# Optimization experiments

Hardware: AMD Instinct MI355X
Metric: run time of the kernel (lower is better)

Reference implementation:

```python
import jax, jax.numpy as jnp
import numpy as np

LAMBD = 100.0

def setup_inputs() -> dict:
    key = jax.random.key(0)
    k1, k2, k3 = jax.random.split(key, 3)
    shape = (4096, 4096)
    resnet_outputs = jax.random.normal(k1, shape, dtype=jnp.float32)
    gru_outputs = jax.random.normal(k2, shape, dtype=jnp.float32)
    target = jax.random.normal(k3, shape, dtype=jnp.float32)
    return {"resnet_outputs": resnet_outputs, "gru_outputs": gru_outputs, "target": target}

def reference(resnet_outputs, gru_outputs, target):
    # L1 loss (mean absolute error)
    l1 = jnp.mean(jnp.abs(resnet_outputs - target))
    # smooth_loss: mean absolute deviation of flattened gru_outputs
    g = gru_outputs.ravel()
    smooth = jnp.mean(jnp.abs(g - jnp.mean(g)))
    return l1 + LAMBD * smooth
```

## Files before the change

kernel.cpp:

```cpp
#include <hip/hip_runtime.h>


typedef float f32x4 __attribute__((ext_vector_type(4)));

#define LAMBD 100.0
#define BLOCK 256
#define PT 8
#define TILE (BLOCK * PT)

__device__ __forceinline__ void block_reduce2(float a, float g, float* oa, float* og) {
    #pragma unroll
    for (int off = 32; off; off >>= 1) {
        a += __shfl_down(a, off);
        g += __shfl_down(g, off);
    }
    __shared__ float la[4], lg[4];
    int w = threadIdx.x >> 6;
    if ((threadIdx.x & 63) == 0) { la[w] = a; lg[w] = g; }
    __syncthreads();
    if (threadIdx.x == 0) {
        float ra = 0.f, rg = 0.f;
        #pragma unroll
        for (int i = 0; i < 4; ++i) { ra += la[i]; rg += lg[i]; }
        *oa = ra; *og = rg;
    }
}

__device__ __forceinline__ int swizzle_bid(int bid, int nb) {
    if ((nb & 7) == 0) {
        int nx = nb >> 3;
        return (bid & 7) * nx + (bid >> 3);
    }
    return bid;
}

__global__ void __launch_bounds__(BLOCK) pass1_kernel(const f32x4* __restrict__ r,
                                                      const f32x4* __restrict__ t,
                                                      const f32x4* __restrict__ g,
                                                      double* __restrict__ ws,
                                                      int n4, int nb) {
    int swz = swizzle_bid(blockIdx.x, nb);
    long base = (long)swz * TILE + threadIdx.x;
    float s_abs = 0.f, s_g = 0.f;

    if ((long)swz * TILE + TILE <= n4) {
        f32x4 rv[PT], tv[PT], gv[PT];
        #pragma unroll
        for (int k = 0; k < PT; ++k) rv[k] = __builtin_nontemporal_load(&r[base + k * BLOCK]);
        #pragma unroll
        for (int k = 0; k < PT; ++k) tv[k] = __builtin_nontemporal_load(&t[base + k * BLOCK]);
        #pragma unroll
        for (int k = 0; k < PT; ++k) gv[k] = g[base + k * BLOCK];
        #pragma unroll
        for (int k = 0; k < PT; ++k) {
            f32x4 d = rv[k] - tv[k];
            s_abs += fabsf(d.x) + fabsf(d.y) + fabsf(d.z) + fabsf(d.w);
            s_g   += (gv[k].x + gv[k].y) + (gv[k].z + gv[k].w);
        }
    } else {
        for (int k = 0; k < PT; ++k) {
            long i = base + (long)k * BLOCK;
            if (i < n4) {
                f32x4 rv = r[i], tv = t[i], gv = g[i];
                s_abs += fabsf(rv.x - tv.x) + fabsf(rv.y - tv.y) +
                         fabsf(rv.z - tv.z) + fabsf(rv.w - tv.w);
                s_g += (gv.x + gv.y) + (gv.z + gv.w);
            }
        }
    }

    float ba, bg;
    block_reduce2(s_abs, s_g, &ba, &bg);
    if (threadIdx.x == 0) {
        ws[swz]      = (double)ba;
        ws[nb + swz] = (double)bg;
    }
}

__global__ void __launch_bounds__(1024) mean_kernel(double* __restrict__ ws, int nb, double inv_n) {
    double v = 0.0;
    for (int i = threadIdx.x; i < nb; i += 1024) v += ws[nb + i];
    #pragma unroll
    for (int off = 32; off; off >>= 1) v += __shfl_down(v, off);
    __shared__ double lds[16];
    int w = threadIdx.x >> 6;
    if ((threadIdx.x & 63) == 0) lds[w] = v;
    __syncthreads();
    if (threadIdx.x == 0) {
        double s = 0.0;
        #pragma unroll
        for (int i = 0; i < 16; ++i) s += lds[i];
        ws[2 * nb] = s * inv_n;
    }
}

__global__ void __launch_bounds__(BLOCK) pass2_kernel(const f32x4* __restrict__ g,
                                                      double* __restrict__ ws,
                                                      int n4, int nb, int p2off) {
    float m = (float)ws[2 * nb];
    int swz = swizzle_bid(blockIdx.x, nb);
    long base = (long)swz * TILE + threadIdx.x;
    float s = 0.f;

    if ((long)swz * TILE + TILE <= n4) {
        f32x4 gv[PT];
        #pragma unroll
        for (int k = 0; k < PT; ++k) gv[k] = g[base + k * BLOCK];
        #pragma unroll
        for (int k = 0; k < PT; ++k) {
            s += fabsf(gv[k].x - m) + fabsf(gv[k].y - m) +
                 fabsf(gv[k].z - m) + fabsf(gv[k].w - m);
        }
    } else {
        for (int k = 0; k < PT; ++k) {
            long i = base + (long)k * BLOCK;
            if (i < n4) {
                f32x4 gv = g[i];
                s += fabsf(gv.x - m) + fabsf(gv.y - m) +
                     fabsf(gv.z - m) + fabsf(gv.w - m);
            }
        }
    }

    float bs, dummy;
    block_reduce2(s, 0.f, &bs, &dummy);
    if (threadIdx.x == 0) ws[p2off + swz] = (double)bs;
}

__global__ void __launch_bounds__(1024) finalize_kernel(const double* __restrict__ ws,
                                                        float* __restrict__ out,
                                                        int nb, int p2off, double inv_n) {
    double a = 0.0, s = 0.0;
    for (int i = threadIdx.x; i < nb; i += 1024) { a += ws[i]; s += ws[p2off + i]; }
    #pragma unroll
    for (int off = 32; off; off >>= 1) {
        a += __shfl_down(a, off);
        s += __shfl_down(s, off);
    }
    __shared__ double la[16], ls[16];
    int w = threadIdx.x >> 6;
    if ((threadIdx.x & 63) == 0) { la[w] = a; ls[w] = s; }
    __syncthreads();
    if (threadIdx.x == 0) {
        double ra = 0.0, rs = 0.0;
        #pragma unroll
        for (int i = 0; i < 16; ++i) { ra += la[i]; rs += ls[i]; }
        out[0] = (float)(ra * inv_n + LAMBD * (rs * inv_n));
    }
}

extern "C" void kernel_launch(void* const* d_in, const int* in_sizes, int n_in,
                              void* d_out, int out_size, void* d_ws, size_t ws_size,
                              hipStream_t stream) {
    const f32x4* r = (const f32x4*)d_in[0];
    const f32x4* g = (const f32x4*)d_in[1];
    const f32x4* t = (const f32x4*)d_in[2];
    float* out = (float*)d_out;
    double* ws = (double*)d_ws;

    int n = in_sizes[0];
    int n4 = n >> 2;
    int nb = (n4 + TILE - 1) / TILE;
    int p2off = 2 * nb + 64;
    double inv_n = 1.0 / (double)n;

    pass1_kernel<<<nb, BLOCK, 0, stream>>>(r, t, g, ws, n4, nb);
    mean_kernel<<<1, 1024, 0, stream>>>(ws, nb, inv_n);
    pass2_kernel<<<nb, BLOCK, 0, stream>>>(g, ws, n4, nb, p2off);
    finalize_kernel<<<1, 1024, 0, stream>>>(ws, out, nb, p2off, inv_n);
}
```

Measured before the change: 198.7 us.

## Fuse four reduction kernels into one cooperative persistent kernel with grid syncs

Replaces the pass1, mean, pass2 and finalize kernels with a single cooperative kernel. It runs a persistent grid sized from the occupancy query times 256 CUs, loops over tiles, and uses grid.sync between phases. Every block computes the mean itself from the workspace partials. This removes three kernel launches and their gaps. The cost is grid-wide barrier overhead and a smaller grid of persistent blocks, so the gru tensor may no longer sit in cache for the second pass in the same way as before.

```diff
diff --git a/kernel.cpp b/kernel.cpp
--- a/kernel.cpp
+++ b/kernel.cpp
@@ -1,5 +1,8 @@
 #include <hip/hip_runtime.h>
+#include <hip/hip_cooperative_groups.h>
 
+
+namespace cg = cooperative_groups;
 
 typedef float f32x4 __attribute__((ext_vector_type(4)));
 
@@ -8,144 +11,134 @@
 #define PT 8
 #define TILE (BLOCK * PT)
 
-__device__ __forceinline__ void block_reduce2(float a, float g, float* oa, float* og) {
-    #pragma unroll
-    for (int off = 32; off; off >>= 1) {
-        a += __shfl_down(a, off);
-        g += __shfl_down(g, off);
+__device__ __forceinline__ int swizzle_tile(int tile, int ntiles) {
+    if ((ntiles & 7) == 0) {
+        int nx = ntiles >> 3;
+        return (tile & 7) * nx + (tile >> 3);
     }
-    __shared__ float la[4], lg[4];
-    int w = threadIdx.x >> 6;
-    if ((threadIdx.x & 63) == 0) { la[w] = a; lg[w] = g; }
-    __syncthreads();
-    if (threadIdx.x == 0) {
-        float ra = 0.f, rg = 0.f;
-        #pragma unroll
-        for (int i = 0; i < 4; ++i) { ra += la[i]; rg += lg[i]; }
-        *oa = ra; *og = rg;
-    }
+    return tile;
 }
 
-__device__ __forceinline__ int swizzle_bid(int bid, int nb) {
-    if ((nb & 7) == 0) {
-        int nx = nb >> 3;
-        return (bid & 7) * nx + (bid >> 3);
-    }
-    return bid;
-}
+__global__ void __launch_bounds__(BLOCK, 8)
+fused_kernel(const f32x4* __restrict__ r, const f32x4* __restrict__ t,
+             const f32x4* __restrict__ g, double* __restrict__ ws,
+             float* __restrict__ out, int n4, int ntiles, double inv_n) {
+    cg::grid_group grid = cg::this_grid();
+    __shared__ float  lfa[4], lfb[4];
+    __shared__ double lda[8];
+    const int nblk = gridDim.x;
+    const int tid  = threadIdx.x;
 
-__global__ void __launch_bounds__(BLOCK) pass1_kernel(const f32x4* __restrict__ r,
-                                                      const f32x4* __restrict__ t,
-                                                      const f32x4* __restrict__ g,
-                                                      double* __restrict__ ws,
-                                                      int n4, int nb) {
-    int swz = swizzle_bid(blockIdx.x, nb);
-    long base = (long)swz * TILE + threadIdx.x;
     float s_abs = 0.f, s_g = 0.f;
-
-    if ((long)swz * TILE + TILE <= n4) {
-        f32x4 rv[PT], tv[PT], gv[PT];
-        #pragma unroll
-        for (int k = 0; k < PT; ++k) rv[k] = __builtin_nontemporal_load(&r[base + k * BLOCK]);
-        #pragma unroll
-        for (int k = 0; k < PT; ++k) tv[k] = __builtin_nontemporal_load(&t[base + k * BLOCK]);
-        #pragma unroll
-        for (int k = 0; k < PT; ++k) gv[k] = g[base + k * BLOCK];
-        #pragma unroll
-        for (int k = 0; k < PT; ++k) {
-            f32x4 d = rv[k] - tv[k];
-            s_abs += fabsf(d.x) + fabsf(d.y) + fabsf(d.z) + fabsf(d.w);
-            s_g   += (gv[k].x + gv[k].y) + (gv[k].z + gv[k].w);
-        }
-    } else {
-        for (int k = 0; k < PT; ++k) {
-            long i = base + (long)k * BLOCK;
-            if (i < n4) {
-                f32x4 rv = r[i], tv = t[i], gv = g[i];
-                s_abs += fabsf(rv.x - tv.x) + fabsf(rv.y - tv.y) +
-                         fabsf(rv.z - tv.z) + fabsf(rv.w - tv.w);
-                s_g += (gv.x + gv.y) + (gv.z + gv.w);
+    for (int tile = blockIdx.x; tile < ntiles; tile += nblk) {
+        int swz = swizzle_tile(tile, ntiles);
+        long base = (long)swz * TILE + tid;
+        if ((long)swz * TILE + TILE <= n4) {
+            f32x4 rv[PT], tv[PT], gv[PT];
+            #pragma unroll
+            for (int k = 0; k < PT; ++k) rv[k] = __builtin_nontemporal_load(&r[base + k * BLOCK]);
+            #pragma unroll
+            for (int k = 0; k < PT; ++k) tv[k] = __builtin_nontemporal_load(&t[base + k * BLOCK]);
+            #pragma unroll
+            for (int k = 0; k < PT; ++k) gv[k] = g[base + k * BLOCK];
+            #pragma unroll
+            for (int k = 0; k < PT; ++k) {
+                f32x4 d = rv[k] - tv[k];
+                s_abs += fabsf(d.x) + fabsf(d.y) + fabsf(d.z) + fabsf(d.w);
+                s_g   += (gv[k].x + gv[k].y) + (gv[k].z + gv[k].w);
+            }
+        } else {
+            for (int k = 0; k < PT; ++k) {
+                long i = base + (long)k * BLOCK;
+                if (i < n4) {
+                    f32x4 rv = r[i], tv = t[i], gv = g[i];
+                    s_abs += fabsf(rv.x - tv.x) + fabsf(rv.y - tv.y) +
+                             fabsf(rv.z - tv.z) + fabsf(rv.w - tv.w);
+                    s_g += (gv.x + gv.y) + (gv.z + gv.w);
+                }
             }
         }
     }
+    #pragma unroll
+    for (int off = 32; off; off >>= 1) {
+        s_abs += __shfl_down(s_abs, off);
+        s_g   += __shfl_down(s_g, off);
+    }
+    if ((tid & 63) == 0) { lfa[tid >> 6] = s_abs; lfb[tid >> 6] = s_g; }
+    __syncthreads();
+    if (tid == 0) {
+        float ba = lfa[0] + lfa[1] + lfa[2] + lfa[3];
+        float bg = lfb[0] + lfb[1] + lfb[2] + lfb[3];
+        ws[blockIdx.x]        = (double)ba;
+        ws[nblk + blockIdx.x] = (double)bg;
+        __threadfence();
+    }
+    grid.sync();
 
-    float ba, bg;
-    block_reduce2(s_abs, s_g, &ba, &bg);
-    if (threadIdx.x == 0) {
-        ws[swz]      = (double)ba;
-        ws[nb + swz] = (double)bg;
-    }
-}
-
-__global__ void __launch_bounds__(1024) mean_kernel(double* __restrict__ ws, int nb, double inv_n) {
     double v = 0.0;
-    for (int i = threadIdx.x; i < nb; i += 1024) v += ws[nb + i];
+    for (int i = tid; i < nblk; i += BLOCK) v += ws[nblk + i];
     #pragma unroll
     for (int off = 32; off; off >>= 1) v += __shfl_down(v, off);
-    __shared__ double lds[16];
-    int w = threadIdx.x >> 6;
-    if ((threadIdx.x & 63) == 0) lds[w] = v;
+    if ((tid & 63) == 0) lda[tid >> 6] = v;
     __syncthreads();
-    if (threadIdx.x == 0) {
-        double s = 0.0;
-        #pragma unroll
-        for (int i = 0; i < 16; ++i) s += lds[i];
-        ws[2 * nb] = s * inv_n;
-    }
-}
+    if (tid == 0) lda[4] = (lda[0] + lda[1] + lda[2] + lda[3]) * inv_n;
+    __syncthreads();
+    const float m = (float)lda[4];
 
-__global__ void __launch_bounds__(BLOCK) pass2_kernel(const f32x4* __restrict__ g,
-                                                      double* __restrict__ ws,
-                                                      int n4, int nb, int p2off) {
-    float m = (float)ws[2 * nb];
-    int swz = swizzle_bid(blockIdx.x, nb);
-    long base = (long)swz * TILE + threadIdx.x;
-    float s = 0.f;
-
-    if ((long)swz * TILE + TILE <= n4) {
-        f32x4 gv[PT];
-        #pragma unroll
-        for (int k = 0; k < PT; ++k) gv[k] = g[base + k * BLOCK];
-        #pragma unroll
-        for (int k = 0; k < PT; ++k) {
-            s += fabsf(gv[k].x - m) + fabsf(gv[k].y - m) +
-                 fabsf(gv[k].z - m) + fabsf(gv[k].w - m);
-        }
-    } else {
-        for (int k = 0; k < PT; ++k) {
-            long i = base + (long)k * BLOCK;
-            if (i < n4) {
-                f32x4 gv = g[i];
-                s += fabsf(gv.x - m) + fabsf(gv.y - m) +
-                     fabsf(gv.z - m) + fabsf(gv.w - m);
+    float s2 = 0.f;
+    for (int tile = blockIdx.x; tile < ntiles; tile += nblk) {
+        int swz = swizzle_tile(tile, ntiles);
+        long base = (long)swz * TILE + tid;
+        if ((long)swz * TILE + TILE <= n4) {
+            f32x4 gv[PT];
+            #pragma unroll
+            for (int k = 0; k < PT; ++k) gv[k] = g[base + k * BLOCK];
+            #pragma unroll
+            for (int k = 0; k < PT; ++k) {
+                s2 += fabsf(gv[k].x - m) + fabsf(gv[k].y - m) +
+                      fabsf(gv[k].z - m) + fabsf(gv[k].w - m);
+            }
+        } else {
+            for (int k = 0; k < PT; ++k) {
+                long i = base + (long)k * BLOCK;
+                if (i < n4) {
+                    f32x4 gv = g[i];
+                    s2 += fabsf(gv.x - m) + fabsf(gv.y - m) +
+                          fabsf(gv.z - m) + fabsf(gv.w - m);
+                }
             }
         }
     }
+    #pragma unroll
+    for (int off = 32; off; off >>= 1) s2 += __shfl_down(s2, off);
+    __syncthreads();
+    if ((tid & 63) == 0) lfa[tid >> 6] = s2;
+    __syncthreads();
+    if (tid == 0) {
+        float bs = lfa[0] + lfa[1] + lfa[2] + lfa[3];
+        ws[2 * nblk + blockIdx.x] = (double)bs;
+        __threadfence();
+    }
+    grid.sync();
 
-    float bs, dummy;
-    block_reduce2(s, 0.f, &bs, &dummy);
-    if (threadIdx.x == 0) ws[p2off + swz] = (double)bs;
-}
-
-__global__ void __launch_bounds__(1024) finalize_kernel(const double* __restrict__ ws,
-                                                        float* __restrict__ out,
-                                                        int nb, int p2off, double inv_n) {
-    double a = 0.0, s = 0.0;
-    for (int i = threadIdx.x; i < nb; i += 1024) { a += ws[i]; s += ws[p2off + i]; }
-    #pragma unroll
-    for (int off = 32; off; off >>= 1) {
-        a += __shfl_down(a, off);
-        s += __shfl_down(s, off);
-    }
-    __shared__ double la[16], ls[16];
-    int w = threadIdx.x >> 6;
-    if ((threadIdx.x & 63) == 0) { la[w] = a; ls[w] = s; }
-    __syncthreads();
-    if (threadIdx.x == 0) {
-        double ra = 0.0, rs = 0.0;
+    if (blockIdx.x == 0) {
+        double a = 0.0, s = 0.0;
+        for (int i = tid; i < nblk; i += BLOCK) {
+            a += ws[i];
+            s += ws[2 * nblk + i];
+        }
         #pragma unroll
-        for (int i = 0; i < 16; ++i) { ra += la[i]; rs += ls[i]; }
-        out[0] = (float)(ra * inv_n + LAMBD * (rs * inv_n));
+        for (int off = 32; off; off >>= 1) {
+            a += __shfl_down(a, off);
+            s += __shfl_down(s, off);
+        }
+        if ((tid & 63) == 0) { lda[tid >> 6] = a; lda[4 + (tid >> 6)] = s; }
+        __syncthreads();
+        if (tid == 0) {
+            double ra = lda[0] + lda[1] + lda[2] + lda[3];
+            double rs = lda[4] + lda[5] + lda[6] + lda[7];
+            out[0] = (float)(ra * inv_n + LAMBD * (rs * inv_n));
+        }
     }
 }
 
@@ -160,12 +153,17 @@
 
     int n = in_sizes[0];
     int n4 = n >> 2;
-    int nb = (n4 + TILE - 1) / TILE;
-    int p2off = 2 * nb + 64;
+    int ntiles = (n4 + TILE - 1) / TILE;
     double inv_n = 1.0 / (double)n;
 
-    pass1_kernel<<<nb, BLOCK, 0, stream>>>(r, t, g, ws, n4, nb);
-    mean_kernel<<<1, 1024, 0, stream>>>(ws, nb, inv_n);
-    pass2_kernel<<<nb, BLOCK, 0, stream>>>(g, ws, n4, nb, p2off);
-    finalize_kernel<<<1, 1024, 0, stream>>>(ws, out, nb, p2off, inv_n);
+    int occ = 8;
+    hipOccupancyMaxActiveBlocksPerMultiprocessor(&occ, (const void*)fused_kernel, BLOCK, 0);
+    if (occ < 1) occ = 1;
+    int grid = occ * 256;
+    if (grid > ntiles) grid = ntiles;
+
+    void* args[] = {(void*)&r, (void*)&t, (void*)&g, (void*)&ws,
+                    (void*)&out, (void*)&n4, (void*)&ntiles, (void*)&inv_n};
+    hipLaunchCooperativeKernel((void*)fused_kernel, dim3(grid), dim3(BLOCK),
+                               args, 0, stream);
 }
```

Measured after the change: 506.9 us. 2.55x slower.
